# Performance work log

Measured on AMD Instinct MI355X. Metric: run time of the kernel, lower is better.

The kernel has to match this reference:

```python
import jax, jax.numpy as jnp
import numpy as np

B, S, I, H = 64, 2048, 64, 128


def setup_inputs() -> dict:
    key = jax.random.key(0)
    ks = jax.random.split(key, 4)
    return {
        'x': jax.random.normal(ks[0], (B, S, I), dtype=jnp.float32),
        'w0': jax.random.normal(ks[1], (I, H), dtype=jnp.float32) * 0.1,
        'u0': jax.random.normal(ks[2], (H, H), dtype=jnp.float32) * 0.1,
        'bg0': jnp.ones((1, H), jnp.float32),
        'bu0': jnp.ones((1, H), jnp.float32),
        'zeta0': jnp.full((1, 1), 1.0, jnp.float32),
        'nu0': jnp.full((1, 1), -4.0, jnp.float32),
        'lambd0': jnp.zeros((1,), jnp.float32),
        'gamma0': jnp.full((1,), 0.999, jnp.float32),
        'w1': jax.random.normal(jax.random.fold_in(key, 10), (H, H), dtype=jnp.float32) * 0.1,
        'u1': jax.random.normal(ks[3], (H, H), dtype=jnp.float32) * 0.1,
        'bg1': jnp.ones((1, H), jnp.float32),
        'bu1': jnp.ones((1, H), jnp.float32),
        'zeta1': jnp.full((1, 1), 1.0, jnp.float32),
        'nu1': jnp.full((1, 1), -4.0, jnp.float32),
        'lambd1': jnp.zeros((1,), jnp.float32),
        'gamma1': jnp.full((1,), 0.999, jnp.float32),
    }


def _layer(x_seq, w, u, bg, bu, zeta, nu, lambd, gamma):
    # x_seq: [B, S, in]; precompute input projection for all timesteps
    wx = jnp.einsum('bsi,ih->bsh', x_seq, w)  # [B, S, H]
    sz = jax.nn.sigmoid(zeta)  # [1,1]
    sn = jax.nn.sigmoid(nu)    # [1,1]
    gc = jnp.clip(gamma, 0.0, 1.0)  # [1]
    h0 = jnp.zeros((x_seq.shape[0], u.shape[0]), x_seq.dtype)

    def step(h, wx_t):
        pre = wx_t + h @ u            # [B, H]
        z = jax.nn.sigmoid(pre + bg)  # gate
        h_hat = jnp.tanh(pre + bu)    # update
        h_new = z * h + (sz * (1.0 - z) + sn) * h_hat
        h_comfi = gc * h_new + (1.0 - gc) * lambd
        return h_comfi, h_comfi

    h_T, outs = jax.lax.scan(step, h0, jnp.swapaxes(wx, 0, 1))  # outs: [S, B, H]
    return jnp.swapaxes(outs, 0, 1), h_T


def reference(x, w0, u0, bg0, bu0, zeta0, nu0, lambd0, gamma0,
              w1, u1, bg1, bu1, zeta1, nu1, lambd1, gamma1):
    out0, h0T = _layer(x, w0, u0, bg0, bu0, zeta0, nu0, lambd0, gamma0)
    out1, h1T = _layer(out0, w1, u1, bg1, bu1, zeta1, nu1, lambd1, gamma1)
    h_n = jnp.stack([h0T, h1T], axis=0)  # [num_layers, B, H]
    return out1, h_n
```

## Files before the change

kernel.cpp:

```cpp
#include <hip/hip_runtime.h>
#include <hip/hip_bf16.h>

#define BB 64
#define SS 2048
#define II 64
#define HH 128
#define CH 64

typedef _Float16 half8 __attribute__((ext_vector_type(8)));
typedef float f32x4 __attribute__((ext_vector_type(4)));

#define LOG2E 1.44269504088896340736f

__device__ __forceinline__ float sigm(float x) { return 1.0f / (1.0f + __expf(-x)); }

__global__ __launch_bounds__(256, 4)
void wx0_kernel(const float* __restrict__ x, const float* __restrict__ w0,
                float* __restrict__ wx0) {
  __shared__ float xs[32][64];
  const int tid = threadIdx.x;
  const int j = tid & (HH - 1);
  const int rh = tid >> 7;
  const long row0 = (long)blockIdx.x * 32;

  float w0c[II];
#pragma unroll
  for (int i = 0; i < II; ++i) w0c[i] = w0[i * HH + j];

  const float4* xg = (const float4*)(x + row0 * II);
  float4* xsv = (float4*)&xs[0][0];
  xsv[tid] = xg[tid];
  xsv[tid + 256] = xg[tid + 256];
  __syncthreads();

#pragma unroll
  for (int rp = 0; rp < 16; ++rp) {
    int r = rp * 2 + rh;
    float acc = 0.f;
#pragma unroll
    for (int i = 0; i < II; i += 4) {
      float4 xv = *(const float4*)&xs[r][i];
      acc += w0c[i] * xv.x + w0c[i + 1] * xv.y + w0c[i + 2] * xv.z +
             w0c[i + 3] * xv.w;
    }
    wx0[(row0 + r) * HH + j] = acc;
  }
}

__global__ __launch_bounds__(256, 1)
void scan_kernel(const float* __restrict__ wx0,
                 const float* __restrict__ u0, const float* __restrict__ bg0,
                 const float* __restrict__ bu0, const float* __restrict__ zeta0,
                 const float* __restrict__ nu0, const float* __restrict__ lambd0,
                 const float* __restrict__ gamma0,
                 const float* __restrict__ w1, const float* __restrict__ u1,
                 const float* __restrict__ bg1, const float* __restrict__ bu1,
                 const float* __restrict__ zeta1, const float* __restrict__ nu1,
                 const float* __restrict__ lambd1, const float* __restrict__ gamma1,
                 float* __restrict__ out1, float* __restrict__ hn) {
  const int b = blockIdx.x;
  const int tid = threadIdx.x;
  const int w = tid >> 6;
  const int l = tid & 63;
  const int g = l >> 4;
  const int n = l & 15;
  const int c0 = 32 * w + n;
  const int c1 = c0 + 16;
  const int parity = g & 1;
  const int colsel = g >> 1;

  half8 wf[3][2][4];
#pragma unroll
  for (int mt = 0; mt < 3; ++mt) {
    const float* W = (mt == 0) ? u0 : (mt == 1) ? w1 : u1;
#pragma unroll
    for (int nt = 0; nt < 2; ++nt) {
      const int col = 32 * w + 16 * nt + n;
#pragma unroll
      for (int kt = 0; kt < 4; ++kt) {
        half8 f;
#pragma unroll
        for (int i = 0; i < 8; ++i) {
          int k = 32 * kt + (i < 4 ? 4 * g + i : 16 + 4 * g + (i - 4));
          f[i] = (_Float16)W[k * HH + col];
        }
        wf[mt][nt][kt] = f;
      }
    }
  }

  const float szg = parity ? sigm(zeta1[0]) : sigm(zeta0[0]);
  const float sng = parity ? sigm(nu1[0]) : sigm(nu0[0]);
  const float gcraw = parity ? gamma1[0] : gamma0[0];
  const float gcg = fminf(fmaxf(gcraw, 0.f), 1.f);
  const float kcg = (1.f - gcg) * (parity ? lambd1[0] : lambd0[0]);
  const float ebg_0 = -LOG2E * (parity ? bg1[c0] : bg0[c0]);
  const float ebg_1 = -LOG2E * (parity ? bg1[c1] : bg0[c1]);
  const float ebu_0 = -2.f * LOG2E * (parity ? bu1[c0] : bu0[c0]);
  const float ebu_1 = -2.f * LOG2E * (parity ? bu1[c1] : bu0[c1]);

  auto gate = [](float pre, float hp, float eg, float eu, float sz, float sn,
                 float gc, float kc) -> float {
    float p  = __builtin_amdgcn_exp2f(__builtin_fmaf(pre, -LOG2E, eg));
    float qq = __builtin_amdgcn_exp2f(__builtin_fmaf(pre, -2.f * LOG2E, eu));
    float opp = 1.f + p, opq = 1.f + qq, omq = 1.f - qq;
    float t1 = __builtin_fmaf(sn, opp, sz * p);
    float num = __builtin_fmaf(hp, opq, t1 * omq);
    float hnew = num * __builtin_amdgcn_rcpf(opp * opq);
    return __builtin_fmaf(gc, hnew, kc);
  };

  __shared__ __align__(16) _Float16 Hpk[2][2][160];
  __shared__ __align__(16) float wxb[CH * HH];

  const float* wxg = wx0 + (size_t)b * SS * HH;
  float* outg = out1 + (size_t)b * SS * HH;

  const int widx = (w * 4 + (n >> 2)) * 8 + (n & 3) + (colsel << 2);
  const int rbase = 8 * g;

  {
    const float4* src = (const float4*)(wxg + HH);
    float4* dst = (float4*)wxb;
#pragma unroll
    for (int i = 0; i < 8; ++i) dst[i * 256 + tid] = src[i * 256 + tid];
  }
  float hp0, hp1;
  {
    const float sz0 = sigm(zeta0[0]), sn0 = sigm(nu0[0]);
    const float gc0 = fminf(fmaxf(gamma0[0], 0.f), 1.f);
    const float kc0 = (1.f - gc0) * lambd0[0];
    float h00 = gate(wxg[c0], 0.f, -LOG2E * bg0[c0], -2.f * LOG2E * bu0[c0],
                     sz0, sn0, gc0, kc0);
    float h01 = gate(wxg[c1], 0.f, -LOG2E * bg0[c1], -2.f * LOG2E * bu0[c1],
                     sz0, sn0, gc0, kc0);
    hp0 = parity ? 0.f : h00;
    hp1 = parity ? 0.f : h01;
    float wv = parity ? 0.f : (colsel ? h01 : h00);
    Hpk[0][parity][widx] = (_Float16)wv;
  }
  asm volatile("s_waitcnt lgkmcnt(0)" ::: "memory");
  __builtin_amdgcn_s_barrier();

  const f32x4 zero = {0.f, 0.f, 0.f, 0.f};

  for (int t = 0; t < SS; ++t) {
    const int rd = t & 1, wr = rd ^ 1;
    const int q = t & (CH - 1);

    half8 a0[4], a1[4];
#pragma unroll
    for (int kt = 0; kt < 4; ++kt) {
      a0[kt] = __builtin_bit_cast(half8,
                 *(const uint4*)&Hpk[rd][0][kt * 32 + rbase]);
      a1[kt] = __builtin_bit_cast(half8,
                 *(const uint4*)&Hpk[rd][1][kt * 32 + rbase]);
    }
    float wxv0 = wxb[q * HH + c0];
    float wxv1 = wxb[q * HH + c1];

    f32x4 accA0, accA1, accB0, accB1, accC0, accC1;
#pragma unroll
    for (int kt = 0; kt < 4; ++kt) {
      accA0 = __builtin_amdgcn_mfma_f32_16x16x32_f16(a0[kt], wf[0][0][kt], kt ? accA0 : zero, 0, 0, 0);
      accA1 = __builtin_amdgcn_mfma_f32_16x16x32_f16(a0[kt], wf[0][1][kt], kt ? accA1 : zero, 0, 0, 0);
      accB0 = __builtin_amdgcn_mfma_f32_16x16x32_f16(a0[kt], wf[1][0][kt], kt ? accB0 : zero, 0, 0, 0);
      accB1 = __builtin_amdgcn_mfma_f32_16x16x32_f16(a0[kt], wf[1][1][kt], kt ? accB1 : zero, 0, 0, 0);
      accC0 = __builtin_amdgcn_mfma_f32_16x16x32_f16(a1[kt], wf[2][0][kt], kt ? accC0 : zero, 0, 0, 0);
      accC1 = __builtin_amdgcn_mfma_f32_16x16x32_f16(a1[kt], wf[2][1][kt], kt ? accC1 : zero, 0, 0, 0);
    }
    float sumA0 = accA0[0], sumA1 = accA1[0];
    float sumB0 = accB0[0], sumB1 = accB1[0];
    float sumC0 = accC0[0], sumC1 = accC1[0];

    float pre_0 = parity ? (sumB0 + sumC0) : (sumA0 + wxv0);
    float pre_1 = parity ? (sumB1 + sumC1) : (sumA1 + wxv1);
    float hc0 = gate(pre_0, hp0, ebg_0, ebu_0, szg, sng, gcg, kcg);
    float hc1 = gate(pre_1, hp1, ebg_1, ebu_1, szg, sng, gcg, kcg);
    hp0 = hc0;
    hp1 = hc1;

    float wval = colsel ? hc1 : hc0;
    Hpk[wr][parity][widx] = (_Float16)wval;
    if (parity) {
      outg[(size_t)t * HH + (colsel ? c1 : c0)] = wval;
      if (t == SS - 1) hn[BB * HH + b * HH + (colsel ? c1 : c0)] = wval;
    } else {
      if (t == SS - 2) hn[b * HH + (colsel ? c1 : c0)] = wval;
    }

    asm volatile("s_waitcnt lgkmcnt(0)" ::: "memory");
    __builtin_amdgcn_s_barrier();

    if (q == CH - 1 && t + 1 < SS) {
      float4* wdst = (float4*)wxb;
#pragma unroll
      for (int i = 0; i < 8; ++i) {
        int flat4 = i * 256 + tid;
        int row = t + 2 + (flat4 >> 5);
        row = row < SS ? row : SS - 1;
        int col4 = flat4 & 31;
        wdst[flat4] = *(const float4*)(wxg + (size_t)row * HH + col4 * 4);
      }
      asm volatile("s_waitcnt lgkmcnt(0)" ::: "memory");
      __builtin_amdgcn_s_barrier();
    }
  }
}

extern "C" void kernel_launch(void* const* d_in, const int* in_sizes, int n_in,
                              void* d_out, int out_size, void* d_ws, size_t ws_size,
                              hipStream_t stream) {
  const float* x      = (const float*)d_in[0];
  const float* w0     = (const float*)d_in[1];
  const float* u0     = (const float*)d_in[2];
  const float* bg0    = (const float*)d_in[3];
  const float* bu0    = (const float*)d_in[4];
  const float* zeta0  = (const float*)d_in[5];
  const float* nu0    = (const float*)d_in[6];
  const float* lambd0 = (const float*)d_in[7];
  const float* gamma0 = (const float*)d_in[8];
  const float* w1     = (const float*)d_in[9];
  const float* u1     = (const float*)d_in[10];
  const float* bg1    = (const float*)d_in[11];
  const float* bu1    = (const float*)d_in[12];
  const float* zeta1  = (const float*)d_in[13];
  const float* nu1    = (const float*)d_in[14];
  const float* lambd1 = (const float*)d_in[15];
  const float* gamma1 = (const float*)d_in[16];

  float* out = (float*)d_out;
  float* hn  = out + (size_t)BB * SS * HH;
  float* wx0 = (float*)d_ws;

  wx0_kernel<<<(BB * SS) / 32, 256, 0, stream>>>(x, w0, wx0);
  scan_kernel<<<BB, 256, 0, stream>>>(wx0, u0, bg0, bu0, zeta0, nu0, lambd0,
                                      gamma0, w1, u1, bg1, bu1, zeta1, nu1,
                                      lambd1, gamma1, out, hn);
}
```

Baseline: 892.8 us.

## Split scan recurrence across 8 waves with one column tile per wave

The scan kernel now launches 512 threads (8 waves), each wave owning one 16-column tile instead of two. Each wave issues 12 MFMAs per step instead of 24, and every lane computes both layer gates for its column. Lane groups are then assigned to LDS writeback, output store and final-state store. This shortens the serial per-step MFMA chain on the critical path. In exchange, each barrier now synchronises more waves and the gate math is duplicated across lanes.

```diff
diff --git a/kernel.cpp b/kernel.cpp
--- a/kernel.cpp
+++ b/kernel.cpp
@@ -47,7 +47,7 @@
   }
 }
 
-__global__ __launch_bounds__(256, 1)
+__global__ __launch_bounds__(512, 1)
 void scan_kernel(const float* __restrict__ wx0,
                  const float* __restrict__ u0, const float* __restrict__ bg0,
                  const float* __restrict__ bu0, const float* __restrict__ zeta0,
@@ -64,40 +64,32 @@
   const int l = tid & 63;
   const int g = l >> 4;
   const int n = l & 15;
-  const int c0 = 32 * w + n;
-  const int c1 = c0 + 16;
-  const int parity = g & 1;
-  const int colsel = g >> 1;
-
-  half8 wf[3][2][4];
-#pragma unroll
-  for (int mt = 0; mt < 3; ++mt) {
-    const float* W = (mt == 0) ? u0 : (mt == 1) ? w1 : u1;
-#pragma unroll
-    for (int nt = 0; nt < 2; ++nt) {
-      const int col = 32 * w + 16 * nt + n;
-#pragma unroll
-      for (int kt = 0; kt < 4; ++kt) {
-        half8 f;
-#pragma unroll
-        for (int i = 0; i < 8; ++i) {
-          int k = 32 * kt + (i < 4 ? 4 * g + i : 16 + 4 * g + (i - 4));
-          f[i] = (_Float16)W[k * HH + col];
-        }
-        wf[mt][nt][kt] = f;
-      }
-    }
-  }
-
-  const float szg = parity ? sigm(zeta1[0]) : sigm(zeta0[0]);
-  const float sng = parity ? sigm(nu1[0]) : sigm(nu0[0]);
-  const float gcraw = parity ? gamma1[0] : gamma0[0];
-  const float gcg = fminf(fmaxf(gcraw, 0.f), 1.f);
-  const float kcg = (1.f - gcg) * (parity ? lambd1[0] : lambd0[0]);
-  const float ebg_0 = -LOG2E * (parity ? bg1[c0] : bg0[c0]);
-  const float ebg_1 = -LOG2E * (parity ? bg1[c1] : bg0[c1]);
-  const float ebu_0 = -2.f * LOG2E * (parity ? bu1[c0] : bu0[c0]);
-  const float ebu_1 = -2.f * LOG2E * (parity ? bu1[c1] : bu0[c1]);
+  const int c = 16 * w + n;
+
+  half8 wfA[4], wfB[4], wfC[4];
+#pragma unroll
+  for (int kt = 0; kt < 4; ++kt) {
+    half8 fa, fb, fc;
+#pragma unroll
+    for (int i = 0; i < 8; ++i) {
+      int k = 32 * kt + (i < 4 ? 4 * g + i : 16 + 4 * g + (i - 4));
+      fa[i] = (_Float16)u0[k * HH + c];
+      fb[i] = (_Float16)w1[k * HH + c];
+      fc[i] = (_Float16)u1[k * HH + c];
+    }
+    wfA[kt] = fa; wfB[kt] = fb; wfC[kt] = fc;
+  }
+
+  const float sz0 = sigm(zeta0[0]), sn0 = sigm(nu0[0]);
+  const float gc0 = fminf(fmaxf(gamma0[0], 0.f), 1.f);
+  const float kc0 = (1.f - gc0) * lambd0[0];
+  const float sz1 = sigm(zeta1[0]), sn1 = sigm(nu1[0]);
+  const float gc1 = fminf(fmaxf(gamma1[0], 0.f), 1.f);
+  const float kc1 = (1.f - gc1) * lambd1[0];
+  const float ebg0 = -LOG2E * bg0[c];
+  const float ebu0 = -2.f * LOG2E * bu0[c];
+  const float ebg1 = -LOG2E * bg1[c];
+  const float ebu1 = -2.f * LOG2E * bu1[c];
 
   auto gate = [](float pre, float hp, float eg, float eu, float sz, float sn,
                  float gc, float kc) -> float {
@@ -116,28 +108,23 @@
   const float* wxg = wx0 + (size_t)b * SS * HH;
   float* outg = out1 + (size_t)b * SS * HH;
 
-  const int widx = (w * 4 + (n >> 2)) * 8 + (n & 3) + (colsel << 2);
+  const int wkt = c >> 5;
+  const int wr_ = c & 31;
+  const int widx = (wkt * 4 + ((wr_ & 15) >> 2)) * 8 + ((wr_ >> 4) << 2) + (wr_ & 3);
   const int rbase = 8 * g;
 
   {
     const float4* src = (const float4*)(wxg + HH);
     float4* dst = (float4*)wxb;
 #pragma unroll
-    for (int i = 0; i < 8; ++i) dst[i * 256 + tid] = src[i * 256 + tid];
-  }
-  float hp0, hp1;
+    for (int i = 0; i < 4; ++i) dst[i * 512 + tid] = src[i * 512 + tid];
+  }
+  float hp0, hp1 = 0.f;
   {
-    const float sz0 = sigm(zeta0[0]), sn0 = sigm(nu0[0]);
-    const float gc0 = fminf(fmaxf(gamma0[0], 0.f), 1.f);
-    const float kc0 = (1.f - gc0) * lambd0[0];
-    float h00 = gate(wxg[c0], 0.f, -LOG2E * bg0[c0], -2.f * LOG2E * bu0[c0],
-                     sz0, sn0, gc0, kc0);
-    float h01 = gate(wxg[c1], 0.f, -LOG2E * bg0[c1], -2.f * LOG2E * bu0[c1],
-                     sz0, sn0, gc0, kc0);
-    hp0 = parity ? 0.f : h00;
-    hp1 = parity ? 0.f : h01;
-    float wv = parity ? 0.f : (colsel ? h01 : h00);
-    Hpk[0][parity][widx] = (_Float16)wv;
+    float h00 = gate(wxg[c], 0.f, ebg0, ebu0, sz0, sn0, gc0, kc0);
+    hp0 = h00;
+    if (g == 0) Hpk[0][0][widx] = (_Float16)h00;
+    if (g == 1) Hpk[0][1][widx] = (_Float16)0.f;
   }
   asm volatile("s_waitcnt lgkmcnt(0)" ::: "memory");
   __builtin_amdgcn_s_barrier();
@@ -145,7 +132,7 @@
   const f32x4 zero = {0.f, 0.f, 0.f, 0.f};
 
   for (int t = 0; t < SS; ++t) {
-    const int rd = t & 1, wr = rd ^ 1;
+    const int rd = t & 1, wb = rd ^ 1;
     const int q = t & (CH - 1);
 
     half8 a0[4], a1[4];
@@ -156,37 +143,29 @@
       a1[kt] = __builtin_bit_cast(half8,
                  *(const uint4*)&Hpk[rd][1][kt * 32 + rbase]);
     }
-    float wxv0 = wxb[q * HH + c0];
-    float wxv1 = wxb[q * HH + c1];
-
-    f32x4 accA0, accA1, accB0, accB1, accC0, accC1;
+    float wxv = wxb[q * HH + c];
+
+    f32x4 accA, accB, accC;
 #pragma unroll
     for (int kt = 0; kt < 4; ++kt) {
-      accA0 = __builtin_amdgcn_mfma_f32_16x16x32_f16(a0[kt], wf[0][0][kt], kt ? accA0 : zero, 0, 0, 0);
-      accA1 = __builtin_amdgcn_mfma_f32_16x16x32_f16(a0[kt], wf[0][1][kt], kt ? accA1 : zero, 0, 0, 0);
-      accB0 = __builtin_amdgcn_mfma_f32_16x16x32_f16(a0[kt], wf[1][0][kt], kt ? accB0 : zero, 0, 0, 0);
-      accB1 = __builtin_amdgcn_mfma_f32_16x16x32_f16(a0[kt], wf[1][1][kt], kt ? accB1 : zero, 0, 0, 0);
-      accC0 = __builtin_amdgcn_mfma_f32_16x16x32_f16(a1[kt], wf[2][0][kt], kt ? accC0 : zero, 0, 0, 0);
-      accC1 = __builtin_amdgcn_mfma_f32_16x16x32_f16(a1[kt], wf[2][1][kt], kt ? accC1 : zero, 0, 0, 0);
-    }
-    float sumA0 = accA0[0], sumA1 = accA1[0];
-    float sumB0 = accB0[0], sumB1 = accB1[0];
-    float sumC0 = accC0[0], sumC1 = accC1[0];
-
-    float pre_0 = parity ? (sumB0 + sumC0) : (sumA0 + wxv0);
-    float pre_1 = parity ? (sumB1 + sumC1) : (sumA1 + wxv1);
-    float hc0 = gate(pre_0, hp0, ebg_0, ebu_0, szg, sng, gcg, kcg);
-    float hc1 = gate(pre_1, hp1, ebg_1, ebu_1, szg, sng, gcg, kcg);
+      accA = __builtin_amdgcn_mfma_f32_16x16x32_f16(a0[kt], wfA[kt], kt ? accA : zero, 0, 0, 0);
+      accB = __builtin_amdgcn_mfma_f32_16x16x32_f16(a0[kt], wfB[kt], kt ? accB : zero, 0, 0, 0);
+      accC = __builtin_amdgcn_mfma_f32_16x16x32_f16(a1[kt], wfC[kt], kt ? accC : zero, 0, 0, 0);
+    }
+
+    float pre0 = accA[0] + wxv;
+    float hc0 = gate(pre0, hp0, ebg0, ebu0, sz0, sn0, gc0, kc0);
     hp0 = hc0;
+    if (g == 0) Hpk[wb][0][widx] = (_Float16)hc0;
+
+    float pre1 = accB[0] + accC[0];
+    float hc1 = gate(pre1, hp1, ebg1, ebu1, sz1, sn1, gc1, kc1);
     hp1 = hc1;
-
-    float wval = colsel ? hc1 : hc0;
-    Hpk[wr][parity][widx] = (_Float16)wval;
-    if (parity) {
-      outg[(size_t)t * HH + (colsel ? c1 : c0)] = wval;
-      if (t == SS - 1) hn[BB * HH + b * HH + (colsel ? c1 : c0)] = wval;
-    } else {
-      if (t == SS - 2) hn[b * HH + (colsel ? c1 : c0)] = wval;
+    if (g == 1) Hpk[wb][1][widx] = (_Float16)hc1;
+    if (g == 2) outg[(size_t)t * HH + c] = hc1;
+    if (g == 3) {
+      if (t == SS - 2) hn[b * HH + c] = hc0;
+      if (t == SS - 1) hn[BB * HH + b * HH + c] = hc1;
     }
 
     asm volatile("s_waitcnt lgkmcnt(0)" ::: "memory");
@@ -195,8 +174,8 @@
     if (q == CH - 1 && t + 1 < SS) {
       float4* wdst = (float4*)wxb;
 #pragma unroll
-      for (int i = 0; i < 8; ++i) {
-        int flat4 = i * 256 + tid;
+      for (int i = 0; i < 4; ++i) {
+        int flat4 = i * 512 + tid;
         int row = t + 2 + (flat4 >> 5);
         row = row < SS ? row : SS - 1;
         int col4 = flat4 & 31;
@@ -234,7 +213,7 @@
   float* wx0 = (float*)d_ws;
 
   wx0_kernel<<<(BB * SS) / 32, 256, 0, stream>>>(x, w0, wx0);
-  scan_kernel<<<BB, 256, 0, stream>>>(wx0, u0, bg0, bu0, zeta0, nu0, lambd0,
+  scan_kernel<<<BB, 512, 0, stream>>>(wx0, u0, bg0, bu0, zeta0, nu0, lambd0,
                                       gamma0, w1, u1, bg1, bu1, zeta1, nu1,
                                       lambd1, gamma1, out, hn);
 }
```

Result: slower. 933.4 us (+4.6%).
